# Performance work log

Hardware: AMD Instinct MI355X
Metric: run time of the kernel (lower is better)

## Reference

```python
import jax, jax.numpy as jnp
import numpy as np

# Module config (init_kwargs)
CIN, COUT, KH, KW = 256, 256, 3, 3
STRIDE, PADDING = 1, 1
T = 64                 # psum chunk size along the reduction (K) axis
NBITS = 8              # saturating accumulator bits (signed)
QMAX = (1 << (NBITS - 1)) - 1   # 127
QMIN = QMAX - (1 << NBITS) + 1  # -128


def setup_inputs() -> dict:
    key = jax.random.key(0)
    k1, k2 = jax.random.split(key)
    x = jax.random.normal(k1, (8, CIN, 56, 56), dtype=jnp.float32)
    # nn.Parameter(torch.rand((N,1)) * 0.001)
    weights = jax.random.uniform(k2, (CIN * COUT * KH * KW, 1), dtype=jnp.float32) * 0.001
    return {"x": x, "weights": weights}


def reference(x, weights):
    B, _, H, W = x.shape
    OH = (H - KH + 2 * PADDING) // STRIDE + 1
    OW = (W - KW + 2 * PADDING) // STRIDE + 1

    w = weights.reshape(COUT, CIN, KH, KW)
    # per-output-channel scaling factor, detached
    scale = jax.lax.stop_gradient(jnp.mean(jnp.abs(w), axis=(1, 2, 3), keepdims=True))
    # binarize with STE: sign(w).detach() - clamp(w).detach() + clamp(w)
    wc = jnp.clip(w, -1.0, 1.0)
    wb = jax.lax.stop_gradient(jnp.sign(w) - wc) + wc

    # unfold (im2col); channel varies slowest -> matches torch.nn.functional.unfold
    patches = jax.lax.conv_general_dilated_patches(
        x, (KH, KW), (STRIDE, STRIDE), [(PADDING, PADDING), (PADDING, PADDING)]
    )  # [B, CIN*KH*KW, OH*OW... (spatial)]
    K = CIN * KH * KW
    L = OH * OW
    A = patches.reshape(B, K, L).transpose(0, 2, 1)  # [B, L, K]
    X = wb.reshape(COUT, K).T                        # [K, COUT]

    pad = (-K) % T
    if pad:
        A = jnp.pad(A, ((0, 0), (0, 0), (0, pad)))
        X = jnp.pad(X, ((0, pad), (0, 0)))
    nT = (K + pad) // T

    A4 = A.reshape(B, L, nT, T)        # chunked reduction axis
    X3 = X.reshape(nT, T, COUT)
    # per-chunk partial sums (satmm_cuda.forward_psum)
    psum = jnp.einsum('blnt,ntc->nblc', A4, X3)  # [nT, B, L, COUT]

    # saturating sequential accumulation: reduce(lambda a,b: clip(a+b, QMIN, QMAX))
    def step(carry, p):
        return jnp.clip(carry + p, QMIN, QMAX), None
    y_flat, _ = jax.lax.scan(step, psum[0], psum[1:])  # [B, L, COUT]

    y = y_flat.transpose(0, 2, 1).reshape(B, COUT, OH, OW)
    y = y * scale.reshape(1, -1, 1, 1)
    # psum returned in the original [B, L, COUT, nT] layout
    return y, psum.transpose(1, 2, 3, 0)
```

## Files before the change

### kernel.cpp

```cpp
#include <hip/hip_runtime.h>
#include <hip/hip_bf16.h>

#define CIN 256
#define COUT 256
#define HW 56
#define BATCH 8
#define L_SPATIAL 3136
#define K_TOTAL 2304
#define NT 36
#define KSTRIDE 2312
#define ATILE_BYTES (16 * KSTRIDE * 2)
#define STAGE_FLOATS 2304
#define LDS_BYTES (ATILE_BYTES + 8 * STAGE_FLOATS * 4)
#define TILES_PER_IMG 196
#define QMAXF 127.0f
#define QMINF -128.0f

typedef short bf16x8 __attribute__((ext_vector_type(8)));
typedef float f32x4 __attribute__((ext_vector_type(4)));

__device__ __forceinline__ void nt_store4(float* p, f32x4 v) {
  __builtin_nontemporal_store(v, reinterpret_cast<f32x4*>(p));
}

__global__ __launch_bounds__(256) void prep_kernel(
    const float* __restrict__ w, unsigned short* __restrict__ bsign,
    float* __restrict__ scale) {
  const int c = blockIdx.x;
  const int t = threadIdx.x;
  const float* row = w + (size_t)c * K_TOTAL;
  unsigned short* out = bsign + (size_t)c * K_TOTAL;
  float acc = 0.0f;
#pragma unroll
  for (int j = 0; j < 9; ++j) {
    const int k = t + 256 * j;
    const float v = row[k];
    acc += __builtin_fabsf(v);
    out[k] = (v > 0.0f) ? (unsigned short)0x3F80
           : ((v < 0.0f) ? (unsigned short)0xBF80 : (unsigned short)0);
  }
#pragma unroll
  for (int o = 32; o > 0; o >>= 1) acc += __shfl_down(acc, o, 64);
  __shared__ float red[4];
  if ((t & 63) == 0) red[t >> 6] = acc;
  __syncthreads();
  if (t == 0) scale[c] = (red[0] + red[1] + red[2] + red[3]) * (1.0f / 2304.0f);
}

__global__ __launch_bounds__(512, 1) void satconv_kernel(
    const float* __restrict__ x, const unsigned short* __restrict__ bsign,
    const float* __restrict__ scale, float* __restrict__ y_out,
    float* __restrict__ psum_out) {
  extern __shared__ char smem[];
  unsigned short* Atile = (unsigned short*)smem;
  float* stage_base = (float*)(smem + ATILE_BYTES);

  const int tid = threadIdx.x;
  const int m_tile = (blockIdx.x & 7) * TILES_PER_IMG + (blockIdx.x >> 3);
  const int m0 = m_tile << 4;

  {
    const int ml = tid & 15;
    const int grp = tid >> 4;
    const int m = m0 + ml;
    const int b = m / L_SPATIAL;
    const int l = m - b * L_SPATIAL;
    const int oh = l / HW;
    const int ow = l - oh * HW;
    const float* xb = x + (size_t)b * (CIN * L_SPATIAL);
    unsigned short* arow = Atile + ml * KSTRIDE;
    for (int r = grp; r < 768; r += 32) {
      const int ci = r / 3;
      const int kh = r - ci * 3;
      const int h = oh + kh - 1;
      const bool hv = ((unsigned)h < (unsigned)HW);
      const float* xr = xb + (ci * HW + h) * HW;
      const int kb = ci * 9 + kh * 3;
#pragma unroll
      for (int kw = 0; kw < 3; ++kw) {
        const int wv = ow + kw - 1;
        float v = 0.0f;
        if (hv && ((unsigned)wv < (unsigned)HW)) v = xr[wv];
        __hip_bfloat16 bv = __float2bfloat16(v);
        arow[kb + kw] = *reinterpret_cast<unsigned short*>(&bv);
      }
    }
  }

  const int lane = tid & 63;
  const int wave = tid >> 6;
  const int cl = lane & 15;
  const int q = lane >> 4;
  const int c0 = wave << 5;
  float* stage = stage_base + wave * STAGE_FLOATS;

  const float sc_s0 = scale[c0 + cl];
  const float sc_s1 = scale[c0 + 16 + cl];

  int base_it[9];
  {
#pragma unroll
    for (int it = 0; it < 9; ++it) {
      const int f = it * 256 + lane * 4;
      const int qq = f / 576;
      const int rem = f - qq * 576;
      const int ci = rem / 36;
      const int n0 = rem - ci * 36;
      base_it[it] = ((m0 + (qq << 2)) * COUT + ci) * NT + n0;
    }
  }

  __syncthreads();

  const unsigned short* aptr = Atile + cl * KSTRIDE + q * 8;
  const int b_img = m0 / L_SPATIAL;
  const int l0 = m0 - b_img * L_SPATIAL;

  for (int s = 0; s < 2; ++s) {
    const int csub0 = c0 + (s << 4);
    const int c = csub0 + cl;
    const unsigned short* bptr = bsign + (size_t)c * K_TOTAL + q * 8;
    f32x4 ps[NT];
    f32x4 sacc = {0.0f, 0.0f, 0.0f, 0.0f};
    const f32x4 zero = {0.0f, 0.0f, 0.0f, 0.0f};
    bf16x8 b0 = *reinterpret_cast<const bf16x8*>(bptr);
    bf16x8 b1 = *reinterpret_cast<const bf16x8*>(bptr + 32);
#pragma unroll
    for (int n = 0; n < NT; ++n) {
      bf16x8 nb0, nb1;
      if (n + 1 < NT) {
        nb0 = *reinterpret_cast<const bf16x8*>(bptr + (n + 1) * 64);
        nb1 = *reinterpret_cast<const bf16x8*>(bptr + (n + 1) * 64 + 32);
      }
      bf16x8 a0 = *reinterpret_cast<const bf16x8*>(aptr + n * 64);
      bf16x8 a1 = *reinterpret_cast<const bf16x8*>(aptr + n * 64 + 32);
      f32x4 acc = __builtin_amdgcn_mfma_f32_16x16x32_bf16(a0, b0, zero, 0, 0, 0);
      acc = __builtin_amdgcn_mfma_f32_16x16x32_bf16(a1, b1, acc, 0, 0, 0);
      ps[n] = acc;
      if (n == 0) {
        sacc = acc;
      } else {
#pragma unroll
        for (int e = 0; e < 4; ++e) {
          const float t = sacc[e] + acc[e];
          sacc[e] = __builtin_amdgcn_fmed3f(t, QMINF, QMAXF);
        }
      }
      b0 = nb0;
      b1 = nb1;
    }

    {
      const float sc = (s == 0) ? sc_s0 : sc_s1;
      f32x4 yv;
#pragma unroll
      for (int e = 0; e < 4; ++e) yv[e] = sacc[e] * sc;
      *reinterpret_cast<f32x4*>(stage + cl * 16 + q * 4) = yv;
      const int ci = lane >> 2;
      const int mi = (lane & 3) << 2;
      f32x4 v = *reinterpret_cast<const f32x4*>(stage + lane * 4);
      nt_store4(y_out + ((size_t)b_img * COUT + (csub0 + ci)) * L_SPATIAL + l0 + mi, v);
    }

    const int soff = csub0 * NT;
#pragma unroll
    for (int rg = 0; rg < 4; ++rg) {
#pragma unroll
      for (int g = 0; g < 9; ++g) {
        f32x4 v = {ps[4 * g + 0][rg], ps[4 * g + 1][rg],
                   ps[4 * g + 2][rg], ps[4 * g + 3][rg]};
        *reinterpret_cast<f32x4*>(stage + q * 576 + cl * 36 + 4 * g) = v;
      }
      const int rgoff = rg * (COUT * NT) + soff;
#pragma unroll
      for (int it = 0; it < 9; ++it) {
        f32x4 v = *reinterpret_cast<const f32x4*>(stage + it * 256 + lane * 4);
        nt_store4(psum_out + (size_t)(base_it[it] + rgoff), v);
      }
    }
  }
}

extern "C" void kernel_launch(void* const* d_in, const int* in_sizes, int n_in,
                              void* d_out, int out_size, void* d_ws, size_t ws_size,
                              hipStream_t stream) {
  const float* x = (const float*)d_in[0];
  const float* w = (const float*)d_in[1];
  float* y = (float*)d_out;
  float* psum = y + (size_t)BATCH * COUT * L_SPATIAL;
  unsigned short* bsign = (unsigned short*)d_ws;
  float* scale = (float*)((char*)d_ws + (size_t)COUT * K_TOTAL * 2);

  prep_kernel<<<COUT, 256, 0, stream>>>(w, bsign, scale);

  hipFuncSetAttribute(reinterpret_cast<const void*>(satconv_kernel),
                      hipFuncAttributeMaxDynamicSharedMemorySize, LDS_BYTES);
  satconv_kernel<<<(BATCH * L_SPATIAL) / 16, 512, LDS_BYTES, stream>>>(
      x, bsign, scale, y, psum);
}
```

Before: 1.187 ms.

## Split im2col into separate kernel writing MFMA-swizzled A tiles to workspace

Moves the im2col gather into its own kernel, which writes bf16 A fragments to global workspace already laid out in MFMA lane order. A separate GEMM kernel then reads A straight from global memory with 4 waves of 256 threads and 64 output channels per wave, using less LDS so two blocks can share a CU. This separates the gather phase from the compute/store phase, but adds a roughly 115 MB workspace write and read-back plus an extra launch. The fused kernel is kept as a fallback when the workspace is too small, and its B-prefetch is removed.

```diff
diff --git a/kernel.cpp b/kernel.cpp
--- a/kernel.cpp
+++ b/kernel.cpp
@@ -11,8 +11,9 @@
 #define KSTRIDE 2312
 #define ATILE_BYTES (16 * KSTRIDE * 2)
 #define STAGE_FLOATS 2304
-#define LDS_BYTES (ATILE_BYTES + 8 * STAGE_FLOATS * 4)
 #define TILES_PER_IMG 196
+#define N_MTILES 1568
+#define ASW_ELEMS_PER_TILE (NT * 2 * 512)
 #define QMAXF 127.0f
 #define QMINF -128.0f
 
@@ -47,6 +48,146 @@
   if (t == 0) scale[c] = (red[0] + red[1] + red[2] + red[3]) * (1.0f / 2304.0f);
 }
 
+__global__ __launch_bounds__(256) void im2col_kernel(
+    const float* __restrict__ x, unsigned short* __restrict__ asw) {
+  extern __shared__ unsigned short Atile[];
+  const int tid = threadIdx.x;
+  const int m_tile = blockIdx.x;
+  const int m0 = m_tile << 4;
+  {
+    const int ml = tid & 15;
+    const int grp = tid >> 4;
+    const int m = m0 + ml;
+    const int b = m / L_SPATIAL;
+    const int l = m - b * L_SPATIAL;
+    const int oh = l / HW;
+    const int ow = l - oh * HW;
+    const float* xb = x + (size_t)b * (CIN * L_SPATIAL);
+    unsigned short* arow = Atile + ml * KSTRIDE;
+    for (int r = grp; r < 768; r += 16) {
+      const int ci = r / 3;
+      const int kh = r - ci * 3;
+      const int h = oh + kh - 1;
+      const bool hv = ((unsigned)h < (unsigned)HW);
+      const float* xr = xb + (ci * HW + h) * HW;
+      const int kb = ci * 9 + kh * 3;
+#pragma unroll
+      for (int kw = 0; kw < 3; ++kw) {
+        const int wv = ow + kw - 1;
+        float v = 0.0f;
+        if (hv && ((unsigned)wv < (unsigned)HW)) v = xr[wv];
+        __hip_bfloat16 bv = __float2bfloat16(v);
+        arow[kb + kw] = *reinterpret_cast<unsigned short*>(&bv);
+      }
+    }
+  }
+  __syncthreads();
+  unsigned short* dst = asw + (size_t)m_tile * ASW_ELEMS_PER_TILE;
+#pragma unroll
+  for (int it = 0; it < 18; ++it) {
+    const int flat = it * 256 + tid;
+    const int n = flat >> 7;
+    const int rem = flat & 127;
+    const int frag = rem >> 6;
+    const int ln = rem & 63;
+    const int cl = ln & 15;
+    const int q = ln >> 4;
+    bf16x8 v = *reinterpret_cast<const bf16x8*>(
+        Atile + cl * KSTRIDE + n * 64 + frag * 32 + q * 8);
+    *reinterpret_cast<bf16x8*>(dst + (size_t)flat * 8) = v;
+  }
+}
+
+__global__ __launch_bounds__(256, 2) void gemm_kernel(
+    const unsigned short* __restrict__ asw, const unsigned short* __restrict__ bsign,
+    const float* __restrict__ scale, float* __restrict__ y_out,
+    float* __restrict__ psum_out) {
+  __shared__ float stage_all[4 * STAGE_FLOATS];
+  const int tid = threadIdx.x;
+  const int m_tile = (blockIdx.x & 7) * TILES_PER_IMG + (blockIdx.x >> 3);
+  const int m0 = m_tile << 4;
+  const int lane = tid & 63;
+  const int wave = tid >> 6;
+  const int cl = lane & 15;
+  const int q = lane >> 4;
+  const int c0 = wave << 6;
+  float* stage = stage_all + wave * STAGE_FLOATS;
+
+  const unsigned short* atile =
+      asw + (size_t)m_tile * ASW_ELEMS_PER_TILE + lane * 8;
+  const int b_img = m0 / L_SPATIAL;
+  const int l0 = m0 - b_img * L_SPATIAL;
+
+  int base_it[9];
+#pragma unroll
+  for (int it = 0; it < 9; ++it) {
+    const int f = it * 256 + lane * 4;
+    const int qq = f / 576;
+    const int rem = f - qq * 576;
+    const int ci = rem / 36;
+    const int n0 = rem - ci * 36;
+    base_it[it] = ((m0 + (qq << 2)) * COUT + ci) * NT + n0;
+  }
+
+  for (int s = 0; s < 4; ++s) {
+    const int csub0 = c0 + (s << 4);
+    const int c = csub0 + cl;
+    const float sc = scale[c];
+    const unsigned short* bptr = bsign + (size_t)c * K_TOTAL + q * 8;
+    f32x4 ps[NT];
+    f32x4 sacc = {0.0f, 0.0f, 0.0f, 0.0f};
+    const f32x4 zero = {0.0f, 0.0f, 0.0f, 0.0f};
+#pragma unroll
+    for (int n = 0; n < NT; ++n) {
+      bf16x8 a0 = *reinterpret_cast<const bf16x8*>(atile + n * 1024);
+      bf16x8 a1 = *reinterpret_cast<const bf16x8*>(atile + n * 1024 + 512);
+      bf16x8 b0 = *reinterpret_cast<const bf16x8*>(bptr + n * 64);
+      bf16x8 b1 = *reinterpret_cast<const bf16x8*>(bptr + n * 64 + 32);
+      f32x4 acc = __builtin_amdgcn_mfma_f32_16x16x32_bf16(a0, b0, zero, 0, 0, 0);
+      acc = __builtin_amdgcn_mfma_f32_16x16x32_bf16(a1, b1, acc, 0, 0, 0);
+      ps[n] = acc;
+      if (n == 0) {
+        sacc = acc;
+      } else {
+#pragma unroll
+        for (int e = 0; e < 4; ++e) {
+          const float t = sacc[e] + acc[e];
+          sacc[e] = __builtin_amdgcn_fmed3f(t, QMINF, QMAXF);
+        }
+      }
+    }
+
+    {
+      f32x4 yv;
+#pragma unroll
+      for (int e = 0; e < 4; ++e) yv[e] = sacc[e] * sc;
+      *reinterpret_cast<f32x4*>(stage + cl * 16 + q * 4) = yv;
+      const int ci = lane >> 2;
+      const int mi = (lane & 3) << 2;
+      f32x4 v = *reinterpret_cast<const f32x4*>(stage + lane * 4);
+      nt_store4(y_out + ((size_t)b_img * COUT + (csub0 + ci)) * L_SPATIAL + l0 + mi, v);
+    }
+
+    const int soff = csub0 * NT;
+#pragma unroll
+    for (int rg = 0; rg < 4; ++rg) {
+#pragma unroll
+      for (int g = 0; g < 9; ++g) {
+        f32x4 v = {ps[4 * g + 0][rg], ps[4 * g + 1][rg],
+                   ps[4 * g + 2][rg], ps[4 * g + 3][rg]};
+        *reinterpret_cast<f32x4*>(stage + q * 576 + cl * 36 + 4 * g) = v;
+      }
+      const int rgoff = rg * (COUT * NT) + soff;
+#pragma unroll
+      for (int it = 0; it < 9; ++it) {
+        f32x4 v = *reinterpret_cast<const f32x4*>(stage + it * 256 + lane * 4);
+        nt_store4(psum_out + (size_t)(base_it[it] + rgoff), v);
+      }
+    }
+  }
+}
+
+#define FB_LDS_BYTES (ATILE_BYTES + 8 * STAGE_FLOATS * 4)
 __global__ __launch_bounds__(512, 1) void satconv_kernel(
     const float* __restrict__ x, const unsigned short* __restrict__ bsign,
     const float* __restrict__ scale, float* __restrict__ y_out,
@@ -54,11 +195,9 @@
   extern __shared__ char smem[];
   unsigned short* Atile = (unsigned short*)smem;
   float* stage_base = (float*)(smem + ATILE_BYTES);
-
   const int tid = threadIdx.x;
   const int m_tile = (blockIdx.x & 7) * TILES_PER_IMG + (blockIdx.x >> 3);
   const int m0 = m_tile << 4;
-
   {
     const int ml = tid & 15;
     const int grp = tid >> 4;
@@ -86,36 +225,28 @@
       }
     }
   }
-
   const int lane = tid & 63;
   const int wave = tid >> 6;
   const int cl = lane & 15;
   const int q = lane >> 4;
   const int c0 = wave << 5;
   float* stage = stage_base + wave * STAGE_FLOATS;
-
   const float sc_s0 = scale[c0 + cl];
   const float sc_s1 = scale[c0 + 16 + cl];
-
   int base_it[9];
-  {
-#pragma unroll
-    for (int it = 0; it < 9; ++it) {
-      const int f = it * 256 + lane * 4;
-      const int qq = f / 576;
-      const int rem = f - qq * 576;
-      const int ci = rem / 36;
-      const int n0 = rem - ci * 36;
-      base_it[it] = ((m0 + (qq << 2)) * COUT + ci) * NT + n0;
-    }
-  }
-
+#pragma unroll
+  for (int it = 0; it < 9; ++it) {
+    const int f = it * 256 + lane * 4;
+    const int qq = f / 576;
+    const int rem = f - qq * 576;
+    const int ci = rem / 36;
+    const int n0 = rem - ci * 36;
+    base_it[it] = ((m0 + (qq << 2)) * COUT + ci) * NT + n0;
+  }
   __syncthreads();
-
   const unsigned short* aptr = Atile + cl * KSTRIDE + q * 8;
   const int b_img = m0 / L_SPATIAL;
   const int l0 = m0 - b_img * L_SPATIAL;
-
   for (int s = 0; s < 2; ++s) {
     const int csub0 = c0 + (s << 4);
     const int c = csub0 + cl;
@@ -123,17 +254,12 @@
     f32x4 ps[NT];
     f32x4 sacc = {0.0f, 0.0f, 0.0f, 0.0f};
     const f32x4 zero = {0.0f, 0.0f, 0.0f, 0.0f};
-    bf16x8 b0 = *reinterpret_cast<const bf16x8*>(bptr);
-    bf16x8 b1 = *reinterpret_cast<const bf16x8*>(bptr + 32);
 #pragma unroll
     for (int n = 0; n < NT; ++n) {
-      bf16x8 nb0, nb1;
-      if (n + 1 < NT) {
-        nb0 = *reinterpret_cast<const bf16x8*>(bptr + (n + 1) * 64);
-        nb1 = *reinterpret_cast<const bf16x8*>(bptr + (n + 1) * 64 + 32);
-      }
       bf16x8 a0 = *reinterpret_cast<const bf16x8*>(aptr + n * 64);
       bf16x8 a1 = *reinterpret_cast<const bf16x8*>(aptr + n * 64 + 32);
+      bf16x8 b0 = *reinterpret_cast<const bf16x8*>(bptr + n * 64);
+      bf16x8 b1 = *reinterpret_cast<const bf16x8*>(bptr + n * 64 + 32);
       f32x4 acc = __builtin_amdgcn_mfma_f32_16x16x32_bf16(a0, b0, zero, 0, 0, 0);
       acc = __builtin_amdgcn_mfma_f32_16x16x32_bf16(a1, b1, acc, 0, 0, 0);
       ps[n] = acc;
@@ -146,10 +272,7 @@
           sacc[e] = __builtin_amdgcn_fmed3f(t, QMINF, QMAXF);
         }
       }
-      b0 = nb0;
-      b1 = nb1;
-    }
-
+    }
     {
       const float sc = (s == 0) ? sc_s0 : sc_s1;
       f32x4 yv;
@@ -161,7 +284,6 @@
       f32x4 v = *reinterpret_cast<const f32x4*>(stage + lane * 4);
       nt_store4(y_out + ((size_t)b_img * COUT + (csub0 + ci)) * L_SPATIAL + l0 + mi, v);
     }
-
     const int soff = csub0 * NT;
 #pragma unroll
     for (int rg = 0; rg < 4; ++rg) {
@@ -190,11 +312,19 @@
   float* psum = y + (size_t)BATCH * COUT * L_SPATIAL;
   unsigned short* bsign = (unsigned short*)d_ws;
   float* scale = (float*)((char*)d_ws + (size_t)COUT * K_TOTAL * 2);
+  unsigned short* asw = (unsigned short*)((char*)d_ws + (2u << 20));
+  const size_t need = (2u << 20) + (size_t)N_MTILES * ASW_ELEMS_PER_TILE * 2;
 
   prep_kernel<<<COUT, 256, 0, stream>>>(w, bsign, scale);
 
-  hipFuncSetAttribute(reinterpret_cast<const void*>(satconv_kernel),
-                      hipFuncAttributeMaxDynamicSharedMemorySize, LDS_BYTES);
-  satconv_kernel<<<(BATCH * L_SPATIAL) / 16, 512, LDS_BYTES, stream>>>(
-      x, bsign, scale, y, psum);
-}
+  if (ws_size >= need) {
+    hipFuncSetAttribute(reinterpret_cast<const void*>(im2col_kernel),
+                        hipFuncAttributeMaxDynamicSharedMemorySize, ATILE_BYTES);
+    im2col_kernel<<<N_MTILES, 256, ATILE_BYTES, stream>>>(x, asw);
+    gemm_kernel<<<N_MTILES, 256, 0, stream>>>(asw, bsign, scale, y, psum);
+  } else {
+    hipFuncSetAttribute(reinterpret_cast<const void*>(satconv_kernel),
+                        hipFuncAttributeMaxDynamicSharedMemorySize, FB_LDS_BYTES);
+    satconv_kernel<<<N_MTILES, 512, FB_LDS_BYTES, stream>>>(x, bsign, scale, y, psum);
+  }
+}
```

After: 1.477 ms. 1.24x slower.
